# Performance work log

Measured on AMD Instinct MI355X. Metric: run time of the kernel, lower is better.

Reference implementation:

```python
import jax, jax.numpy as jnp
import numpy as np

D = 160          # volume side
WIN = 32         # spatial window size (box filter, matches fftconvolve with ones kernel)
NUM_MIN = 100    # minimum count constraint (constraint.min_number_from_ratio)
K_CCL = 16       # fixed number of 6-neighbor min-propagation sweeps (CCL definition)
NUM_BINS = 4096  # fixed histogram bins replacing data-dependent np.unique
VALUES = (0, 1, 2)
LIST_LABELS = (1,)
NUM_LABELS = 2
HALF = WIN // 2


def _box1d(x, w, ax):
    # 'same' box-sum along one axis via cumsum (== fftconvolve with ones(w))
    left = w // 2
    right = w - 1 - left
    x = jnp.moveaxis(x, ax, -1)
    pads = [(0, 0)] * (x.ndim - 1) + [(left, right)]
    c = jnp.cumsum(jnp.pad(x, pads), axis=-1)
    c = jnp.pad(c, [(0, 0)] * (x.ndim - 1) + [(1, 0)])
    out = c[..., w:] - c[..., :-w]
    return jnp.moveaxis(out, -1, ax)


def box_sum(x, w):
    for ax in range(x.ndim):
        x = _box1d(x, w, ax)
    return x


def _shift(a, s, ax, fill):
    # shift by s along ax, filling vacated border with `fill`
    r = jnp.roll(a, s, axis=ax)
    n = a.shape[ax]
    co = jnp.arange(n).reshape([n if i == ax else 1 for i in range(a.ndim)])
    bad = (co < s) if s > 0 else (co >= n + s)
    return jnp.where(bad, fill, r)


def label_size_map(seg):
    # create_label_size_map: connected-component labeling (6-connectivity,
    # K_CCL min-propagation sweeps) then replace each component by its size.
    n_vox = seg.size
    big = jnp.int32(n_vox + 2)
    idx = (jnp.arange(n_vox, dtype=jnp.int32) + 1).reshape(seg.shape)
    lab0 = jnp.where(seg, idx, big)

    def step(_, lab):
        m = lab
        for ax in range(seg.ndim):
            for s in (1, -1):
                m = jnp.minimum(m, _shift(lab, s, ax, big))
        return jnp.where(seg, m, big)

    lab = jax.lax.fori_loop(0, K_CCL, step, lab0)
    labels = jnp.where(seg, lab, 0)  # background -> label 0
    cnt = jnp.zeros(n_vox + 1, jnp.float32).at[labels.ravel()].add(1.0)
    return jnp.where(seg, cnt[labels], 0.0)


def _proba_weights(candidates, mean_list):
    # create_probability_weights: reciprocal-histogram weighting over rounded
    # mean component sizes (fixed NUM_BINS integer bins; bin 0 = non-candidate).
    pw = jnp.ones_like(candidates)
    for m in mean_list:
        possible = candidates * m
        idx = jnp.clip(jnp.round(possible), 0, NUM_BINS - 1).astype(jnp.int32)
        hist = jnp.zeros(NUM_BINS, jnp.float32).at[idx.ravel()].add(1.0)
        numb = jnp.sum(hist[1:])
        rec = jnp.where(hist[1:] > 0, numb / jnp.maximum(hist[1:], 1.0), 0.0)
        ph = rec / jnp.sum(rec)
        ph_full = jnp.concatenate([jnp.zeros(1, jnp.float32), ph])
        pw = pw * ph_full[idx]
    return pw / jnp.sum(pw)


def setup_inputs() -> dict:
    key = jax.random.key(0)
    data = jax.random.randint(key, (D, D, D), 0, 3).astype(jnp.float32)
    return {"data": data}


def reference(data):
    data = jnp.round(data)
    inner = tuple(s - 2 * HALF for s in data.shape)
    final = jnp.pad(jnp.ones(inner, jnp.float32), [(HALF, HALF)] * 3)
    mean_list = []
    valid_others = []
    for v in VALUES:
        seg = data == v
        segf = seg.astype(jnp.float32)
        lsize = label_size_map(seg)
        cw = box_sum(segf, WIN)                              # counts_window
        valid = (cw > max(NUM_MIN, 1)).astype(jnp.float32)   # valid_places
        cs = box_sum(lsize * valid, WIN)                     # counts_size
        mean = jnp.where(cw > 0, cs / jnp.maximum(cw, 1.0), 0.0)
        if v in LIST_LABELS:
            mean_list.append(mean)
            final = final * valid
        else:
            valid_others.append(valid)
    for vo in valid_others:
        final = final + vo
    num_labels_add = max(NUM_LABELS - len(LIST_LABELS), 0)
    candidates = (final >= num_labels_add + 1).astype(jnp.float32)
    proba_fin = _proba_weights(candidates, mean_list)
    return candidates, proba_fin
```

## Files before the change

### kernel.cpp

```cpp
#include <hip/hip_runtime.h>
#include <cmath>

#define D 160
#define DD (D*D)
#define NVOX (D*D*D)
#define BIGV (NVOX + 2)
#define NBINS 4096
#define HALF 16
#define RGRID 800
#define SGRID 1000

template<int MODE>
__global__ __launch_bounds__(256) void box_rot_int_kernel(
    const void* __restrict__ vin, unsigned* __restrict__ out)
{
    __shared__ unsigned tin[32][161];
    __shared__ unsigned filt[160][33];
    int L0 = blockIdx.x * 32;
    size_t base = (size_t)L0 * D;

    if (MODE == 0) {
        const float4* s4 = (const float4*)((const float*)vin + base);
        for (int i = threadIdx.x; i < 32 * (D / 4); i += 256) {
            float4 v = s4[i];
            int e = i * 4, r = e / D, c = e - r * D;
            float rr;
            rr = rintf(v.x); tin[r][c]   = (rr==0.f) | ((rr==1.f)?0x10000u:0u);
            rr = rintf(v.y); tin[r][c+1] = (rr==0.f) | ((rr==1.f)?0x10000u:0u);
            rr = rintf(v.z); tin[r][c+2] = (rr==0.f) | ((rr==1.f)?0x10000u:0u);
            rr = rintf(v.w); tin[r][c+3] = (rr==0.f) | ((rr==1.f)?0x10000u:0u);
        }
    } else {
        const uint4* s4 = (const uint4*)((const unsigned*)vin + base);
        for (int i = threadIdx.x; i < 32 * (D / 4); i += 256) {
            uint4 v = s4[i];
            int e = i * 4, r = e / D, c = e - r * D;
            tin[r][c] = v.x; tin[r][c+1] = v.y; tin[r][c+2] = v.z; tin[r][c+3] = v.w;
        }
    }
    __syncthreads();

    {
        int r = threadIdx.x & 31, s = threadIdx.x >> 5;
        int i0 = 20 * s;
        const unsigned* ln = tin[r];
        unsigned sum = 0u;
        int jlo = i0 - 16; if (jlo < 0) jlo = 0;
        int jhi = i0 + 15; if (jhi > D - 1) jhi = D - 1;
        for (int j = jlo; j <= jhi; ++j) sum += ln[j];
        #pragma unroll 4
        for (int k = 0; k < 20; ++k) {
            int i = i0 + k;
            filt[i][r] = sum;
            int add = i + 16, rem = i - 16;
            if (add <= D - 1) sum += ln[add];
            if (rem >= 0)     sum -= ln[rem];
        }
    }
    __syncthreads();

    int r = threadIdx.x & 31;
    for (int c = (threadIdx.x >> 5); c < D; c += 8)
        out[(size_t)c * DD + L0 + r] = filt[c][r];
}

__global__ __launch_bounds__(256) void box_rot_f32_g_kernel(
    const int* __restrict__ lab, const int* __restrict__ cnt,
    const unsigned* __restrict__ cwp, float* __restrict__ out)
{
    __shared__ float tin[32][161];
    __shared__ float filt[160][33];
    int L0 = blockIdx.x * 32;
    size_t base = (size_t)L0 * D;

    const int4*  lab4 = (const int4*)(lab + base);
    const uint4* cw4  = (const uint4*)(cwp + base);
    for (int i = threadIdx.x; i < 32 * (D / 4); i += 256) {
        int4 l = lab4[i];
        uint4 cw = cw4[i];
        int e = i * 4, r = e / D, c = e - r * D;
        tin[r][c]   = (l.x != BIGV && (cw.x >> 16) > 100u) ? (float)cnt[l.x] : 0.f;
        tin[r][c+1] = (l.y != BIGV && (cw.y >> 16) > 100u) ? (float)cnt[l.y] : 0.f;
        tin[r][c+2] = (l.z != BIGV && (cw.z >> 16) > 100u) ? (float)cnt[l.z] : 0.f;
        tin[r][c+3] = (l.w != BIGV && (cw.w >> 16) > 100u) ? (float)cnt[l.w] : 0.f;
    }
    __syncthreads();

    {
        int r = threadIdx.x & 31, s = threadIdx.x >> 5;
        int i0 = 20 * s;
        const float* ln = tin[r];
        float sum = 0.f;
        int jlo = i0 - 16; if (jlo < 0) jlo = 0;
        int jhi = i0 + 15; if (jhi > D - 1) jhi = D - 1;
        for (int j = jlo; j <= jhi; ++j) sum += ln[j];
        #pragma unroll 4
        for (int k = 0; k < 20; ++k) {
            int i = i0 + k;
            filt[i][r] = sum;
            int add = i + 16, rem = i - 16;
            if (add <= D - 1) sum += ln[add];
            if (rem >= 0)     sum -= ln[rem];
        }
    }
    __syncthreads();

    int r = threadIdx.x & 31;
    for (int c = (threadIdx.x >> 5); c < D; c += 8)
        out[(size_t)c * DD + L0 + r] = filt[c][r];
}

__global__ __launch_bounds__(256) void box_rot_f32_kernel(
    const float* __restrict__ fin, float* __restrict__ out)
{
    __shared__ float tin[32][161];
    __shared__ float filt[160][33];
    int L0 = blockIdx.x * 32;
    size_t base = (size_t)L0 * D;

    const float4* s4 = (const float4*)(fin + base);
    for (int i = threadIdx.x; i < 32 * (D / 4); i += 256) {
        float4 v = s4[i];
        int e = i * 4, r = e / D, c = e - r * D;
        tin[r][c] = v.x; tin[r][c+1] = v.y; tin[r][c+2] = v.z; tin[r][c+3] = v.w;
    }
    __syncthreads();

    {
        int r = threadIdx.x & 31, s = threadIdx.x >> 5;
        int i0 = 20 * s;
        const float* ln = tin[r];
        float sum = 0.f;
        int jlo = i0 - 16; if (jlo < 0) jlo = 0;
        int jhi = i0 + 15; if (jhi > D - 1) jhi = D - 1;
        for (int j = jlo; j <= jhi; ++j) sum += ln[j];
        #pragma unroll 4
        for (int k = 0; k < 20; ++k) {
            int i = i0 + k;
            filt[i][r] = sum;
            int add = i + 16, rem = i - 16;
            if (add <= D - 1) sum += ln[add];
            if (rem >= 0)     sum -= ln[rem];
        }
    }
    __syncthreads();

    int r = threadIdx.x & 31;
    for (int c = (threadIdx.x >> 5); c < D; c += 8)
        out[(size_t)c * DD + L0 + r] = filt[c][r];
}

__global__ __launch_bounds__(256) void box_rot_fin_kernel(
    const float* __restrict__ fin, const unsigned* __restrict__ cwp,
    float* __restrict__ cand, unsigned short* __restrict__ idxbuf,
    int* __restrict__ partial)
{
    __shared__ float tin[32][161];
    __shared__ float filt[160][33];
    __shared__ int lh[NBINS];
    for (int i = threadIdx.x; i < NBINS; i += 256) lh[i] = 0;

    int L0 = blockIdx.x * 32;
    size_t base = (size_t)L0 * D;
    const float4* s4 = (const float4*)(fin + base);
    for (int i = threadIdx.x; i < 32 * (D / 4); i += 256) {
        float4 v = s4[i];
        int e = i * 4, r = e / D, c = e - r * D;
        tin[r][c] = v.x; tin[r][c+1] = v.y; tin[r][c+2] = v.z; tin[r][c+3] = v.w;
    }
    __syncthreads();

    {
        int r = threadIdx.x & 31, s = threadIdx.x >> 5;
        int i0 = 20 * s;
        const float* ln = tin[r];
        float sum = 0.f;
        int jlo = i0 - 16; if (jlo < 0) jlo = 0;
        int jhi = i0 + 15; if (jhi > D - 1) jhi = D - 1;
        for (int j = jlo; j <= jhi; ++j) sum += ln[j];
        #pragma unroll 4
        for (int k = 0; k < 20; ++k) {
            int i = i0 + k;
            filt[i][r] = sum;
            int add = i + 16, rem = i - 16;
            if (add <= D - 1) sum += ln[add];
            if (rem >= 0)     sum -= ln[rem];
        }
    }
    __syncthreads();

    int r = threadIdx.x & 31;
    int L = L0 + r;
    int y = L / D, z = L - (L / D) * D;
    bool byz = (y >= HALF && y < D - HALF && z >= HALF && z < D - HALF);
    int wy = min(y + 15, D - 1) - max(y - 16, 0) + 1;
    int wz = min(z + 15, D - 1) - max(z - 16, 0) + 1;
    for (int c = (threadIdx.x >> 5); c < D; c += 8) {
        int p = c * DD + L;
        unsigned pk = cwp[p];
        unsigned cw0 = pk & 0xFFFFu;
        unsigned cw1 = pk >> 16;
        int wx = min(c + 15, D - 1) - max(c - 16, 0) + 1;
        unsigned cw2 = (unsigned)(wx * wy * wz) - cw0 - cw1;
        float v0 = (cw0 > 100u) ? 1.f : 0.f;
        float v1 = (cw1 > 100u) ? 1.f : 0.f;
        float v2 = (cw2 > 100u) ? 1.f : 0.f;
        float border = (byz && c >= HALF && c < D - HALF) ? 1.f : 0.f;
        float cd = (border * v1 + v0 + v2 >= 2.f) ? 1.f : 0.f;
        cand[p] = cd;
        float mean = (cw1 > 0u) ? filt[c][r] / fmaxf((float)cw1, 1.f) : 0.f;
        int idx = (int)rintf(cd * mean);
        idx = min(max(idx, 0), NBINS - 1);
        idxbuf[p] = (unsigned short)idx;
        if (idx != 0) atomicAdd(&lh[idx], 1);
    }
    __syncthreads();
    int* po = partial + blockIdx.x * NBINS;
    for (int i = threadIdx.x; i < NBINS; i += 256) po[i] = lh[i];
}

__device__ __forceinline__ int min6(int c, int a, int b, int d, int e, int f, int g) {
    if (c == BIGV) return BIGV;
    return min(min(min(c, a), min(b, d)), min(min(e, f), g));
}

__device__ __forceinline__ int4 min7_run(int4 c, int lm, int rm,
                                         int4 ym, int4 yp, int4 xm, int4 xp) {
    int4 o;
    o.x = min6(c.x, lm,  c.y, ym.x, yp.x, xm.x, xp.x);
    o.y = min6(c.y, c.x, c.z, ym.y, yp.y, xm.y, xp.y);
    o.z = min6(c.z, c.y, c.w, ym.z, yp.z, xm.z, xp.z);
    o.w = min6(c.w, c.z, rm,  ym.w, yp.w, xm.w, xp.w);
    return o;
}

__device__ __forceinline__ void wave_count(int l, int lane, int* __restrict__ cnt) {
    unsigned long long remaining = __ballot(l != BIGV);
    while (remaining) {
        int leader = __ffsll((unsigned long long)remaining) - 1;
        int ll = __shfl(l, leader, 64);
        unsigned long long mm = __ballot(l == ll);
        if (lane == leader) atomicAdd(&cnt[ll], (int)__popcll(mm & remaining));
        remaining &= ~mm;
    }
}

__device__ __forceinline__ int4 cls4(float4 v, int p0) {
    int4 l;
    l.x = (rintf(v.x) == 1.f) ? (p0 + 1) : BIGV;
    l.y = (rintf(v.y) == 1.f) ? (p0 + 2) : BIGV;
    l.z = (rintf(v.z) == 1.f) ? (p0 + 3) : BIGV;
    l.w = (rintf(v.w) == 1.f) ? (p0 + 4) : BIGV;
    return l;
}

struct LabLd {
    const int* __restrict__ a;
    __device__ __forceinline__ int4 v(int p) const { return ((const int4*)a)[p >> 2]; }
    __device__ __forceinline__ int  s(int p) const { return a[p]; }
};
struct DataLd {
    const float* __restrict__ a;
    __device__ __forceinline__ int4 v(int p) const { return cls4(((const float4*)a)[p >> 2], p); }
    __device__ __forceinline__ int  s(int p) const { return (rintf(a[p]) == 1.f) ? (p + 1) : BIGV; }
};

template<typename LD>
__device__ __forceinline__ int4 fused2_chunk(LD ld, int p, int lane)
{
    const int4 BIG4 = make_int4(BIGV, BIGV, BIGV, BIGV);
    int z0 = p % D;
    int rr = p / D;
    int yy = rr % D;
    int xx = rr / D;
    bool gyp = yy < D - 1, gym = yy > 0, gxp = xx < D - 1, gxm = xx > 0;

    int4 C  = ld.v(p);
    int4 Yp = gyp ? ld.v(p + D)  : BIG4;
    int4 Ym = gym ? ld.v(p - D)  : BIG4;
    int4 Xp = gxp ? ld.v(p + DD) : BIG4;
    int4 Xm = gxm ? ld.v(p - DD) : BIG4;

    bool lz = (z0 == 0), rz = (z0 == D - 4);
    bool l0  = (lane == 0)  && !lz;
    bool l63 = (lane == 63) && !rz;
    int lmC  = __shfl_up(C.w, 1),  rmC  = __shfl_down(C.x, 1);
    int lmYp = __shfl_up(Yp.w, 1), rmYp = __shfl_down(Yp.x, 1);
    int lmYm = __shfl_up(Ym.w, 1), rmYm = __shfl_down(Ym.x, 1);
    int lmXp = __shfl_up(Xp.w, 1), rmXp = __shfl_down(Xp.x, 1);
    int lmXm = __shfl_up(Xm.w, 1), rmXm = __shfl_down(Xm.x, 1);
    if (lz) { lmC = lmYp = lmYm = lmXp = lmXm = BIGV; }
    if (rz) { rmC = rmYp = rmYm = rmXp = rmXm = BIGV; }
    if (l0) {
        lmC  = ld.s(p - 1);
        lmYp = gyp ? ld.s(p + D - 1)  : BIGV;
        lmYm = gym ? ld.s(p - D - 1)  : BIGV;
        lmXp = gxp ? ld.s(p + DD - 1) : BIGV;
        lmXm = gxm ? ld.s(p - DD - 1) : BIGV;
    }
    if (l63) {
        rmC  = ld.s(p + 4);
        rmYp = gyp ? ld.s(p + D + 4)  : BIGV;
        rmYm = gym ? ld.s(p - D + 4)  : BIGV;
        rmXp = gxp ? ld.s(p + DD + 4) : BIGV;
        rmXm = gxm ? ld.s(p - DD + 4) : BIGV;
    }

    int4 g1C = min7_run(C, lmC, rmC, Ym, Yp, Xm, Xp);

    int4 Yp2 = (yy < D - 2)  ? ld.v(p + 2 * D)  : BIG4;
    int4 Dpp = (gxp && gyp)  ? ld.v(p + DD + D) : BIG4;
    int4 Dmp = (gxm && gyp)  ? ld.v(p - DD + D) : BIG4;
    int4 g1Yp = min7_run(Yp, lmYp, rmYp, C, Yp2, Dmp, Dpp);

    int4 Ym2 = (yy > 1)      ? ld.v(p - 2 * D)  : BIG4;
    int4 Dpm = (gxp && gym)  ? ld.v(p + DD - D) : BIG4;
    int4 Dmm = (gxm && gym)  ? ld.v(p - DD - D) : BIG4;
    int4 g1Ym = min7_run(Ym, lmYm, rmYm, Ym2, C, Dmm, Dpm);

    int4 Xp2 = (xx < D - 2)  ? ld.v(p + 2 * DD) : BIG4;
    int4 g1Xp = min7_run(Xp, lmXp, rmXp, Dpm, Dpp, C, Xp2);

    int4 Xm2 = (xx > 1)      ? ld.v(p - 2 * DD) : BIG4;
    int4 g1Xm = min7_run(Xm, lmXm, rmXm, Dmm, Dmp, Xm2, C);

    int lmG = __shfl_up(g1C.w, 1), rmG = __shfl_down(g1C.x, 1);
    if (lz) lmG = BIGV;
    if (rz) rmG = BIGV;
    if (l0) {
        lmG = min6(lmC, ld.s(p - 2), C.x, lmYp, lmYm, lmXp, lmXm);
    }
    if (l63) {
        rmG = min6(rmC, C.w, ld.s(p + 5), rmYp, rmYm, rmXp, rmXm);
    }

    return min7_run(g1C, lmG, rmG, g1Ym, g1Yp, g1Xm, g1Xp);
}

__global__ __launch_bounds__(512) void ccl_fused2_data_kernel(
    const float* __restrict__ data, int* __restrict__ outp)
{
    int b = blockIdx.x;
    int sb = (b & 7) * (SGRID / 8) + (b >> 3);
    int lane = threadIdx.x & 63;
    int wv   = threadIdx.x >> 6;
    int wbase = sb * 4096 + wv * 512;
    int pA = wbase + 4 * lane;
    int pB = pA + 256;

    DataLd ld{data};
    int4 oA = fused2_chunk(ld, pA, lane);
    int4 oB = fused2_chunk(ld, pB, lane);

    int4* out4 = (int4*)outp;
    out4[pA >> 2] = oA; out4[pB >> 2] = oB;
}

template<int COUNT>
__global__ __launch_bounds__(512) void ccl_fused2_kernel(
    const int* __restrict__ lab, int* __restrict__ outp, int* __restrict__ cnt)
{
    int b = blockIdx.x;
    int sb = (b & 7) * (SGRID / 8) + (b >> 3);
    int lane = threadIdx.x & 63;
    int wv   = threadIdx.x >> 6;
    int wbase = sb * 4096 + wv * 512;
    int pA = wbase + 4 * lane;
    int pB = pA + 256;

    LabLd ld{lab};
    int4 oA = fused2_chunk(ld, pA, lane);
    int4 oB = fused2_chunk(ld, pB, lane);

    int4* out4 = (int4*)outp;
    out4[pA >> 2] = oA; out4[pB >> 2] = oB;

    if (COUNT) {
        wave_count(oA.x, lane, cnt);
        wave_count(oA.y, lane, cnt);
        wave_count(oA.z, lane, cnt);
        wave_count(oA.w, lane, cnt);
        wave_count(oB.x, lane, cnt);
        wave_count(oB.y, lane, cnt);
        wave_count(oB.z, lane, cnt);
        wave_count(oB.w, lane, cnt);
    }
}

__global__ __launch_bounds__(256) void hist_reduce_kernel(
    const int* __restrict__ partial, int* __restrict__ hist)
{
    int bin = blockIdx.x * 256 + threadIdx.x;
    int s = 0;
    #pragma unroll 4
    for (int b = 0; b < RGRID; ++b) s += partial[b * NBINS + bin];
    hist[bin] = s;
}

__global__ __launch_bounds__(256) void hist_post_kernel(
    const int* __restrict__ hist, float* __restrict__ ph_full,
    float* __restrict__ Sout)
{
    __shared__ float red[256];
    int t = threadIdx.x;

    float loc = 0.f;
    for (int b = t; b < NBINS; b += 256)
        if (b >= 1) loc += (float)hist[b];
    red[t] = loc; __syncthreads();
    for (int o = 128; o > 0; o >>= 1) { if (t < o) red[t] += red[t + o]; __syncthreads(); }
    float numb = red[0]; __syncthreads();

    loc = 0.f;
    for (int b = t; b < NBINS; b += 256) {
        float r = 0.f;
        if (b >= 1) {
            int h = hist[b];
            if (h > 0) r = numb / (float)h;
        }
        ph_full[b] = r;
        loc += r;
    }
    red[t] = loc; __syncthreads();
    for (int o = 128; o > 0; o >>= 1) { if (t < o) red[t] += red[t + o]; __syncthreads(); }
    float sumrec = red[0]; __syncthreads();
    float inv_sumrec = (sumrec > 0.f) ? 1.f / sumrec : 0.f;

    loc = 0.f;
    for (int b = t; b < NBINS; b += 256) {
        float ph = (b >= 1) ? ph_full[b] * inv_sumrec : 0.f;
        ph_full[b] = ph;
        loc += ph * (float)hist[b];
    }
    red[t] = loc; __syncthreads();
    for (int o = 128; o > 0; o >>= 1) { if (t < o) red[t] += red[t + o]; __syncthreads(); }
    if (t == 0) Sout[0] = (red[0] > 0.f) ? red[0] : 1.f;
}

__global__ __launch_bounds__(256) void proba_kernel(
    const unsigned short* __restrict__ idxbuf,
    const float* __restrict__ ph_full, const float* __restrict__ Sv,
    float* __restrict__ outp)
{
    int t = blockIdx.x * blockDim.x + threadIdx.x;
    ushort4 i4 = ((const ushort4*)idxbuf)[t];
    float inv = 1.f / Sv[0];
    float4 o;
    o.x = ph_full[i4.x] * inv;
    o.y = ph_full[i4.y] * inv;
    o.z = ph_full[i4.z] * inv;
    o.w = ph_full[i4.w] * inv;
    ((float4*)outp)[t] = o;
}

extern "C" void kernel_launch(void* const* d_in, const int* in_sizes, int n_in,
                              void* d_out, int out_size, void* d_ws, size_t ws_size,
                              hipStream_t stream)
{
    const float* data = (const float*)d_in[0];
    float* out   = (float*)d_out;
    float* cand  = out;
    float* proba = out + NVOX;

    char* ws = (char*)d_ws;
    const size_t NB = (size_t)NVOX * sizeof(float);
    float* W1 = (float*)(ws);
    float* W2 = (float*)(ws + NB);
    float* W3 = (float*)(ws + 2 * NB);
    int*   cnt  = (int*)(ws + 3 * NB);
    float* ph   = (float*)(ws + 4 * NB + 16);
    int*   hist = (int*)  (ws + 4 * NB + 16 + NBINS * 4);
    float* Sv   = (float*)(ws + 4 * NB + 16 + 2 * NBINS * 4);
    unsigned short* idxbuf = (unsigned short*)cnt;
    int* partial = (int*)W2;

    dim3 rb(256), rg(RGRID);
    dim3 sbk(512), sg(SGRID);
    dim3 pb(256), pg(NVOX / 4 / 256);

    hipMemsetAsync(cnt, 0, (NVOX + 1) * sizeof(int), stream);

    box_rot_int_kernel<0><<<rg, rb, 0, stream>>>(data, (unsigned*)W1);
    box_rot_int_kernel<1><<<rg, rb, 0, stream>>>(W1, (unsigned*)W3);
    box_rot_int_kernel<1><<<rg, rb, 0, stream>>>(W3, (unsigned*)W1);
    unsigned* cwp = (unsigned*)W1;

    ccl_fused2_data_kernel<<<sg, sbk, 0, stream>>>(data, (int*)W2);
    ccl_fused2_kernel<0><<<sg, sbk, 0, stream>>>((int*)W2, (int*)W3, nullptr);
    ccl_fused2_kernel<0><<<sg, sbk, 0, stream>>>((int*)W3, (int*)W2, nullptr);
    ccl_fused2_kernel<0><<<sg, sbk, 0, stream>>>((int*)W2, (int*)W3, nullptr);
    ccl_fused2_kernel<0><<<sg, sbk, 0, stream>>>((int*)W3, (int*)W2, nullptr);
    ccl_fused2_kernel<0><<<sg, sbk, 0, stream>>>((int*)W2, (int*)W3, nullptr);
    ccl_fused2_kernel<0><<<sg, sbk, 0, stream>>>((int*)W3, (int*)W2, nullptr);
    ccl_fused2_kernel<1><<<sg, sbk, 0, stream>>>((int*)W2, (int*)W3, cnt);
    int* lab = (int*)W3;

    box_rot_f32_g_kernel<<<rg, rb, 0, stream>>>(lab, cnt, cwp, W2);
    box_rot_f32_kernel<<<rg, rb, 0, stream>>>(W2, W3);
    box_rot_fin_kernel<<<rg, rb, 0, stream>>>(W3, cwp, cand, idxbuf, partial);

    hist_reduce_kernel<<<dim3(16), dim3(256), 0, stream>>>(partial, hist);
    hist_post_kernel<<<1, 256, 0, stream>>>(hist, ph, Sv);
    proba_kernel<<<pg, pb, 0, stream>>>(idxbuf, ph, Sv, proba);
}
```

Baseline: 482.7 us.

## Co-schedule box-filter passes with single-step CCL sweeps in merged launches

The two-step fused CCL kernel is replaced by a single-step sweep, so the sweep count goes from 8 launches of 2 steps to 16 launches of 1 step. The first three sweeps share a launch with the three box-sum rotation passes, and a fourth sweep shares a launch with zeroing of the count buffer, which replaces the memset. Rotation blocks are widened to 512 threads so they fit the merged grids. The aim is to overlap independent work and drop the redundant neighbour recomputation of the two-step scheme. The cost is twice as many full-volume read and write passes for the CCL and extra kernel launches.

```diff
diff --git a/kernel.cpp b/kernel.cpp
--- a/kernel.cpp
+++ b/kernel.cpp
@@ -9,19 +9,20 @@
 #define HALF 16
 #define RGRID 800
 #define SGRID 1000
+#define ZGRID 1000
 
 template<int MODE>
-__global__ __launch_bounds__(256) void box_rot_int_kernel(
-    const void* __restrict__ vin, unsigned* __restrict__ out)
+__device__ __forceinline__ void rot_block(
+    const void* __restrict__ vin, unsigned* __restrict__ out, int bi, int tid)
 {
     __shared__ unsigned tin[32][161];
     __shared__ unsigned filt[160][33];
-    int L0 = blockIdx.x * 32;
+    int L0 = bi * 32;
     size_t base = (size_t)L0 * D;
 
     if (MODE == 0) {
         const float4* s4 = (const float4*)((const float*)vin + base);
-        for (int i = threadIdx.x; i < 32 * (D / 4); i += 256) {
+        for (int i = tid; i < 32 * (D / 4); i += 512) {
             float4 v = s4[i];
             int e = i * 4, r = e / D, c = e - r * D;
             float rr;
@@ -32,7 +33,7 @@
         }
     } else {
         const uint4* s4 = (const uint4*)((const unsigned*)vin + base);
-        for (int i = threadIdx.x; i < 32 * (D / 4); i += 256) {
+        for (int i = tid; i < 32 * (D / 4); i += 512) {
             uint4 v = s4[i];
             int e = i * 4, r = e / D, c = e - r * D;
             tin[r][c] = v.x; tin[r][c+1] = v.y; tin[r][c+2] = v.z; tin[r][c+3] = v.w;
@@ -41,15 +42,15 @@
     __syncthreads();
 
     {
-        int r = threadIdx.x & 31, s = threadIdx.x >> 5;
-        int i0 = 20 * s;
+        int r = tid & 31, s = tid >> 5;
+        int i0 = 10 * s;
         const unsigned* ln = tin[r];
         unsigned sum = 0u;
         int jlo = i0 - 16; if (jlo < 0) jlo = 0;
         int jhi = i0 + 15; if (jhi > D - 1) jhi = D - 1;
         for (int j = jlo; j <= jhi; ++j) sum += ln[j];
-        #pragma unroll 4
-        for (int k = 0; k < 20; ++k) {
+        #pragma unroll
+        for (int k = 0; k < 10; ++k) {
             int i = i0 + k;
             filt[i][r] = sum;
             int add = i + 16, rem = i - 16;
@@ -59,8 +60,8 @@
     }
     __syncthreads();
 
-    int r = threadIdx.x & 31;
-    for (int c = (threadIdx.x >> 5); c < D; c += 8)
+    int r = tid & 31;
+    for (int c = (tid >> 5); c < D; c += 16)
         out[(size_t)c * DD + L0 + r] = filt[c][r];
 }
 
@@ -265,112 +266,49 @@
     __device__ __forceinline__ int  s(int p) const { return (rintf(a[p]) == 1.f) ? (p + 1) : BIGV; }
 };
 
-template<typename LD>
-__device__ __forceinline__ int4 fused2_chunk(LD ld, int p, int lane)
+template<typename LDT, int COUNT>
+__device__ __forceinline__ void sweep_block(
+    LDT ld, int* __restrict__ outp, int* __restrict__ cnt, int b, int tid)
 {
     const int4 BIG4 = make_int4(BIGV, BIGV, BIGV, BIGV);
-    int z0 = p % D;
-    int rr = p / D;
-    int yy = rr % D;
-    int xx = rr / D;
-    bool gyp = yy < D - 1, gym = yy > 0, gxp = xx < D - 1, gxm = xx > 0;
-
-    int4 C  = ld.v(p);
-    int4 Yp = gyp ? ld.v(p + D)  : BIG4;
-    int4 Ym = gym ? ld.v(p - D)  : BIG4;
-    int4 Xp = gxp ? ld.v(p + DD) : BIG4;
-    int4 Xm = gxm ? ld.v(p - DD) : BIG4;
-
-    bool lz = (z0 == 0), rz = (z0 == D - 4);
-    bool l0  = (lane == 0)  && !lz;
-    bool l63 = (lane == 63) && !rz;
-    int lmC  = __shfl_up(C.w, 1),  rmC  = __shfl_down(C.x, 1);
-    int lmYp = __shfl_up(Yp.w, 1), rmYp = __shfl_down(Yp.x, 1);
-    int lmYm = __shfl_up(Ym.w, 1), rmYm = __shfl_down(Ym.x, 1);
-    int lmXp = __shfl_up(Xp.w, 1), rmXp = __shfl_down(Xp.x, 1);
-    int lmXm = __shfl_up(Xm.w, 1), rmXm = __shfl_down(Xm.x, 1);
-    if (lz) { lmC = lmYp = lmYm = lmXp = lmXm = BIGV; }
-    if (rz) { rmC = rmYp = rmYm = rmXp = rmXm = BIGV; }
-    if (l0) {
-        lmC  = ld.s(p - 1);
-        lmYp = gyp ? ld.s(p + D - 1)  : BIGV;
-        lmYm = gym ? ld.s(p - D - 1)  : BIGV;
-        lmXp = gxp ? ld.s(p + DD - 1) : BIGV;
-        lmXm = gxm ? ld.s(p - DD - 1) : BIGV;
-    }
-    if (l63) {
-        rmC  = ld.s(p + 4);
-        rmYp = gyp ? ld.s(p + D + 4)  : BIGV;
-        rmYm = gym ? ld.s(p - D + 4)  : BIGV;
-        rmXp = gxp ? ld.s(p + DD + 4) : BIGV;
-        rmXm = gxm ? ld.s(p - DD + 4) : BIGV;
-    }
-
-    int4 g1C = min7_run(C, lmC, rmC, Ym, Yp, Xm, Xp);
-
-    int4 Yp2 = (yy < D - 2)  ? ld.v(p + 2 * D)  : BIG4;
-    int4 Dpp = (gxp && gyp)  ? ld.v(p + DD + D) : BIG4;
-    int4 Dmp = (gxm && gyp)  ? ld.v(p - DD + D) : BIG4;
-    int4 g1Yp = min7_run(Yp, lmYp, rmYp, C, Yp2, Dmp, Dpp);
-
-    int4 Ym2 = (yy > 1)      ? ld.v(p - 2 * D)  : BIG4;
-    int4 Dpm = (gxp && gym)  ? ld.v(p + DD - D) : BIG4;
-    int4 Dmm = (gxm && gym)  ? ld.v(p - DD - D) : BIG4;
-    int4 g1Ym = min7_run(Ym, lmYm, rmYm, Ym2, C, Dmm, Dpm);
-
-    int4 Xp2 = (xx < D - 2)  ? ld.v(p + 2 * DD) : BIG4;
-    int4 g1Xp = min7_run(Xp, lmXp, rmXp, Dpm, Dpp, C, Xp2);
-
-    int4 Xm2 = (xx > 1)      ? ld.v(p - 2 * DD) : BIG4;
-    int4 g1Xm = min7_run(Xm, lmXm, rmXm, Dmm, Dmp, Xm2, C);
-
-    int lmG = __shfl_up(g1C.w, 1), rmG = __shfl_down(g1C.x, 1);
-    if (lz) lmG = BIGV;
-    if (rz) rmG = BIGV;
-    if (l0) {
-        lmG = min6(lmC, ld.s(p - 2), C.x, lmYp, lmYm, lmXp, lmXm);
-    }
-    if (l63) {
-        rmG = min6(rmC, C.w, ld.s(p + 5), rmYp, rmYm, rmXp, rmXm);
-    }
-
-    return min7_run(g1C, lmG, rmG, g1Ym, g1Yp, g1Xm, g1Xp);
-}
-
-__global__ __launch_bounds__(512) void ccl_fused2_data_kernel(
-    const float* __restrict__ data, int* __restrict__ outp)
-{
-    int b = blockIdx.x;
     int sb = (b & 7) * (SGRID / 8) + (b >> 3);
-    int lane = threadIdx.x & 63;
-    int wv   = threadIdx.x >> 6;
+    int lane = tid & 63;
+    int wv   = tid >> 6;
     int wbase = sb * 4096 + wv * 512;
     int pA = wbase + 4 * lane;
     int pB = pA + 256;
 
-    DataLd ld{data};
-    int4 oA = fused2_chunk(ld, pA, lane);
-    int4 oB = fused2_chunk(ld, pB, lane);
-
-    int4* out4 = (int4*)outp;
-    out4[pA >> 2] = oA; out4[pB >> 2] = oB;
-}
-
-template<int COUNT>
-__global__ __launch_bounds__(512) void ccl_fused2_kernel(
-    const int* __restrict__ lab, int* __restrict__ outp, int* __restrict__ cnt)
-{
-    int b = blockIdx.x;
-    int sb = (b & 7) * (SGRID / 8) + (b >> 3);
-    int lane = threadIdx.x & 63;
-    int wv   = threadIdx.x >> 6;
-    int wbase = sb * 4096 + wv * 512;
-    int pA = wbase + 4 * lane;
-    int pB = pA + 256;
-
-    LabLd ld{lab};
-    int4 oA = fused2_chunk(ld, pA, lane);
-    int4 oB = fused2_chunk(ld, pB, lane);
+    int4 cA = ld.v(pA), cB = ld.v(pB);
+
+    int zA = pA % D, zB = pB % D;
+    int lmA = __shfl_up(cA.w, 1);
+    int rmA = __shfl_down(cA.x, 1);
+    int lmB = __shfl_up(cB.w, 1);
+    int rmB = __shfl_down(cB.x, 1);
+    int stA = __shfl(cB.x, 0, 64);
+    int stB = __shfl(cA.w, 63, 64);
+    if (lane == 63) rmA = stA;
+    if (lane == 0)  lmB = stB;
+    if (zA == 0)          lmA = BIGV;
+    else if (lane == 0)   lmA = ld.s(pA - 1);
+    if (zA == D - 4)      rmA = BIGV;
+    if (zB == 0)          lmB = BIGV;
+    if (zB == D - 4)      rmB = BIGV;
+    else if (lane == 63)  rmB = ld.s(pB + 4);
+
+    int rA = pA / D, yA = rA % D, xA = rA / D;
+    int4 ylA = (yA > 0)     ? ld.v(pA - D)  : BIG4;
+    int4 yhA = (yA < D - 1) ? ld.v(pA + D)  : BIG4;
+    int4 xlA = (xA > 0)     ? ld.v(pA - DD) : BIG4;
+    int4 xhA = (xA < D - 1) ? ld.v(pA + DD) : BIG4;
+    int4 oA = min7_run(cA, lmA, rmA, ylA, yhA, xlA, xhA);
+
+    int rB = pB / D, yB = rB % D, xB = rB / D;
+    int4 ylB = (yB > 0)     ? ld.v(pB - D)  : BIG4;
+    int4 yhB = (yB < D - 1) ? ld.v(pB + D)  : BIG4;
+    int4 xlB = (xB > 0)     ? ld.v(pB - DD) : BIG4;
+    int4 xhB = (xB < D - 1) ? ld.v(pB + DD) : BIG4;
+    int4 oB = min7_run(cB, lmB, rmB, ylB, yhB, xlB, xhB);
 
     int4* out4 = (int4*)outp;
     out4[pA >> 2] = oA; out4[pB >> 2] = oB;
@@ -387,6 +325,55 @@
     }
 }
 
+__global__ __launch_bounds__(512) void ccl_sweep_kernel(
+    const int* __restrict__ lab, int* __restrict__ outp)
+{
+    LabLd ld{lab};
+    sweep_block<LabLd, 0>(ld, outp, nullptr, blockIdx.x, threadIdx.x);
+}
+
+__global__ __launch_bounds__(512) void ccl_sweep_count_kernel(
+    const int* __restrict__ lab, int* __restrict__ outp, int* __restrict__ cnt)
+{
+    LabLd ld{lab};
+    sweep_block<LabLd, 1>(ld, outp, cnt, blockIdx.x, threadIdx.x);
+}
+
+template<int MODE>
+__global__ __launch_bounds__(512) void sweep_rot_kernel(
+    const float* __restrict__ data, const int* __restrict__ labsrc,
+    int* __restrict__ swdst,
+    const void* __restrict__ rin, unsigned* __restrict__ rout)
+{
+    if ((int)blockIdx.x < SGRID) {
+        if (MODE == 0) {
+            DataLd ld{data};
+            sweep_block<DataLd, 0>(ld, swdst, nullptr, blockIdx.x, threadIdx.x);
+        } else {
+            LabLd ld{labsrc};
+            sweep_block<LabLd, 0>(ld, swdst, nullptr, blockIdx.x, threadIdx.x);
+        }
+    } else {
+        rot_block<MODE>(rin, rout, blockIdx.x - SGRID, threadIdx.x);
+    }
+}
+
+__global__ __launch_bounds__(512) void sweep_zero_kernel(
+    const int* __restrict__ labsrc, int* __restrict__ swdst,
+    int* __restrict__ zbuf)
+{
+    if ((int)blockIdx.x < SGRID) {
+        LabLd ld{labsrc};
+        sweep_block<LabLd, 0>(ld, swdst, nullptr, blockIdx.x, threadIdx.x);
+    } else {
+        int zb = blockIdx.x - SGRID;
+        int t = (zb * 512 + threadIdx.x) * 2;
+        const int4 z4 = make_int4(0, 0, 0, 0);
+        ((int4*)zbuf)[t] = z4; ((int4*)zbuf)[t + 1] = z4;
+        if (zb == 0 && threadIdx.x == 0) zbuf[NVOX] = 0;
+    }
+}
+
 __global__ __launch_bounds__(256) void hist_reduce_kernel(
     const int* __restrict__ partial, int* __restrict__ hist)
 {
@@ -467,7 +454,8 @@
     float* W1 = (float*)(ws);
     float* W2 = (float*)(ws + NB);
     float* W3 = (float*)(ws + 2 * NB);
-    int*   cnt  = (int*)(ws + 3 * NB);
+    int*   W4 = (int*)(ws + 3 * NB);
+    int*   cnt  = W4;
     float* ph   = (float*)(ws + 4 * NB + 16);
     int*   hist = (int*)  (ws + 4 * NB + 16 + NBINS * 4);
     float* Sv   = (float*)(ws + 4 * NB + 16 + 2 * NBINS * 4);
@@ -475,24 +463,28 @@
     int* partial = (int*)W2;
 
     dim3 rb(256), rg(RGRID);
-    dim3 sbk(512), sg(SGRID);
+    dim3 sbk(512);
+    dim3 sg(SGRID);
+    dim3 srg(SGRID + RGRID);
+    dim3 szg(SGRID + ZGRID);
     dim3 pb(256), pg(NVOX / 4 / 256);
 
-    hipMemsetAsync(cnt, 0, (NVOX + 1) * sizeof(int), stream);
-
-    box_rot_int_kernel<0><<<rg, rb, 0, stream>>>(data, (unsigned*)W1);
-    box_rot_int_kernel<1><<<rg, rb, 0, stream>>>(W1, (unsigned*)W3);
-    box_rot_int_kernel<1><<<rg, rb, 0, stream>>>(W3, (unsigned*)W1);
+    sweep_rot_kernel<0><<<srg, sbk, 0, stream>>>(data, nullptr, (int*)W2,
+                                                 data, (unsigned*)W1);
+    sweep_rot_kernel<1><<<srg, sbk, 0, stream>>>(nullptr, (int*)W2, W4,
+                                                 W1, (unsigned*)W3);
+    sweep_rot_kernel<1><<<srg, sbk, 0, stream>>>(nullptr, W4, (int*)W2,
+                                                 W3, (unsigned*)W1);
     unsigned* cwp = (unsigned*)W1;
 
-    ccl_fused2_data_kernel<<<sg, sbk, 0, stream>>>(data, (int*)W2);
-    ccl_fused2_kernel<0><<<sg, sbk, 0, stream>>>((int*)W2, (int*)W3, nullptr);
-    ccl_fused2_kernel<0><<<sg, sbk, 0, stream>>>((int*)W3, (int*)W2, nullptr);
-    ccl_fused2_kernel<0><<<sg, sbk, 0, stream>>>((int*)W2, (int*)W3, nullptr);
-    ccl_fused2_kernel<0><<<sg, sbk, 0, stream>>>((int*)W3, (int*)W2, nullptr);
-    ccl_fused2_kernel<0><<<sg, sbk, 0, stream>>>((int*)W2, (int*)W3, nullptr);
-    ccl_fused2_kernel<0><<<sg, sbk, 0, stream>>>((int*)W3, (int*)W2, nullptr);
-    ccl_fused2_kernel<1><<<sg, sbk, 0, stream>>>((int*)W2, (int*)W3, cnt);
+    sweep_zero_kernel<<<szg, sbk, 0, stream>>>((int*)W2, (int*)W3, W4);
+
+    for (int i = 0; i < 11; ++i) {
+        const int* src = (i & 1) ? (int*)W2 : (int*)W3;
+        int*       dst = (i & 1) ? (int*)W3 : (int*)W2;
+        ccl_sweep_kernel<<<sg, sbk, 0, stream>>>(src, dst);
+    }
+    ccl_sweep_count_kernel<<<sg, sbk, 0, stream>>>((int*)W2, (int*)W3, cnt);
     int* lab = (int*)W3;
 
     box_rot_f32_g_kernel<<<rg, rb, 0, stream>>>(lab, cnt, cwp, W2);
```

After: 391.0 us. 1.23x faster.
